# Kernel tuning notes

Hardware: AMD Instinct MI355X
Metric: run time of the kernel (lower is better)

The kernel has to match this reference:

```python
import jax, jax.numpy as jnp
import numpy as np

D = 1024      # model_size
H = 16        # n_heads
HD = D // H   # head_size
B = 8
S = 1024


def setup_inputs() -> dict:
    key = jax.random.key(0)
    ks = jax.random.split(key, 8)
    sq = lambda k, shp: jax.random.normal(k, shp, dtype=jnp.float32) * (1.0 / np.sqrt(shp[0]))
    return {
        "query": jax.random.normal(ks[0], (B, S, D), dtype=jnp.float32),
        "value": jax.random.normal(ks[1], (B, S, D), dtype=jnp.float32),
        "Wq": sq(ks[2], (D, D)),
        "bq": jnp.zeros((D,), dtype=jnp.float32),
        "Wkv": sq(ks[3], (D, 2 * D)),
        "bkv": jnp.zeros((2 * D,), dtype=jnp.float32),
        "Wo": sq(ks[4], (D, D)),
        "bo": jnp.zeros((D,), dtype=jnp.float32),
    }


def reference(query, value, Wq, bq, Wkv, bkv, Wo, bo):
    scale = 1.0 / jnp.sqrt(jnp.float32(HD))
    q = query @ Wq + bq                      # [B,S,D]
    kv = value @ Wkv + bkv                   # [B,S,2D]
    # tf.split(kv, 2H): chunks 0..H-1 are K heads, H..2H-1 are V heads
    k = kv[..., :D].reshape(B, S, H, HD)
    v = kv[..., D:].reshape(B, S, H, HD)
    qh = q.reshape(B, S, H, HD)
    scores = jnp.einsum("bqhd,bkhd->bhqk", qh, k) * scale   # [B,H,S,S]
    attn = jax.nn.softmax(scores, axis=-1)
    heads = jnp.einsum("bhqk,bkhd->bqhd", attn, v).reshape(B, S, D)
    return heads @ Wo + bo
```

## Files before the change

kernel.cpp:

```cpp
#include <hip/hip_runtime.h>
#include <math.h>

#define B_  8
#define S_  1024
#define D_  1024
#define H_  16
#define HD_ 64

typedef float          floatx4  __attribute__((ext_vector_type(4)));
typedef __bf16         bf16x8   __attribute__((ext_vector_type(8)));
typedef unsigned int   uintx2   __attribute__((ext_vector_type(2)));
typedef unsigned int   uintx4   __attribute__((ext_vector_type(4)));

__device__ __forceinline__ unsigned short f2bf(float f) {
    union { float f; unsigned u; } v; v.f = f;
    unsigned r = v.u + 0x7FFFu + ((v.u >> 16) & 1u);
    return (unsigned short)(r >> 16);
}
__device__ __forceinline__ unsigned pk2(float a, float b) {
    union { __bf16 h[2]; unsigned u; } r;
    r.h[0] = (__bf16)a; r.h[1] = (__bf16)b;
    return r.u;
}
__device__ __forceinline__ void async16(const void* g, void* l) {
    __builtin_amdgcn_global_load_lds(
        (__attribute__((address_space(1))) void*)g,
        (__attribute__((address_space(3))) void*)l, 16, 0, 0);
}

__global__ __launch_bounds__(256) void prep_k(const float* __restrict__ query,
                                              const float* __restrict__ value,
                                              unsigned short* __restrict__ qbf,
                                              unsigned short* __restrict__ vbf,
                                              const float* __restrict__ Wq,
                                              const float* __restrict__ Wkv,
                                              const float* __restrict__ Wo,
                                              unsigned short* __restrict__ WqT,
                                              unsigned short* __restrict__ WkvT,
                                              unsigned short* __restrict__ WoT) {
    __shared__ float T[64 * 68];
    const int t   = threadIdx.x;
    const int bid = blockIdx.x;
    if (bid < 8192) {
        int i = bid * 256 + t;
        floatx4 a = ((const floatx4*)query)[i];
        floatx4 b = ((const floatx4*)value)[i];
        uintx2 oa = { pk2(a[0], a[1]), pk2(a[2], a[3]) };
        uintx2 ob = { pk2(b[0], b[1]), pk2(b[2], b[3]) };
        ((uintx2*)qbf)[i] = oa;
        ((uintx2*)vbf)[i] = ob;
        return;
    }
    const int lin = bid - 8192;
    const int z   = lin >> 8;
    const float* W; unsigned short* WT; int Ndim, nbase;
    if (z == 0)      { W = Wq;  WT = WqT;  Ndim = 1024; nbase = 0; }
    else if (z == 3) { W = Wo;  WT = WoT;  Ndim = 1024; nbase = 0; }
    else             { W = Wkv; WT = WkvT; Ndim = 2048; nbase = (z - 1) * 1024; }
    const int n0 = (lin & 15) * 64 + nbase;
    const int k0 = ((lin >> 4) & 15) * 64;
#pragma unroll
    for (int rep = 0; rep < 4; ++rep) {
        int kl = (t >> 4) + rep * 16;
        int ns = (t & 15) * 4;
        *(floatx4*)(T + kl * 68 + ns) = *(const floatx4*)(W + (size_t)(k0 + kl) * Ndim + n0 + ns);
    }
    __syncthreads();
#pragma unroll
    for (int rep = 0; rep < 2; ++rep) {
        int nl = (t >> 3) + rep * 32;
        int ks = (t & 7) * 8;
        union { unsigned short s[8]; uintx4 u; } o;
#pragma unroll
        for (int j = 0; j < 8; ++j) o.s[j] = f2bf(T[(ks + j) * 68 + nl]);
        *(uintx4*)(WT + (size_t)(n0 + nl) * 1024 + k0 + ks) = o.u;
    }
}

template<int SWAP>
__device__ __forceinline__ void kloop(const unsigned short* __restrict__ ga0,
                                      const unsigned short* __restrict__ gb0,
                                      unsigned short* __restrict__ As,
                                      unsigned short* __restrict__ Bs,
                                      floatx4 (&acc)[4][4],
                                      int w, int lane) {
    const int quad = lane >> 4;
    const int l15  = lane & 15;
    const int e7   = l15 & 7;
    const int wr   = (w >> 1) * 64;
    const int wc   = (w & 1) * 64;
    for (int k0 = 0; k0 < 1024; k0 += 64) {
        if (k0) __syncthreads();
#pragma unroll
        for (int i = 0; i < 4; ++i) {
            int c = i * 4 + w;
            async16(ga0 + (size_t)(c * 8) * 1024 + k0, As + c * 512);
            async16(gb0 + (size_t)(c * 8) * 1024 + k0, Bs + c * 512);
        }
        __syncthreads();
#pragma unroll
        for (int ks = 0; ks < 2; ++ks) {
            bf16x8 af[4], bf[4];
#pragma unroll
            for (int mi = 0; mi < 4; ++mi)
                af[mi] = *(const bf16x8*)(As + (wr + mi * 16 + l15) * 64 + (((ks * 4 + quad) ^ e7) * 8));
#pragma unroll
            for (int ni = 0; ni < 4; ++ni)
                bf[ni] = *(const bf16x8*)(Bs + (wc + ni * 16 + l15) * 64 + (((ks * 4 + quad) ^ e7) * 8));
#pragma unroll
            for (int mi = 0; mi < 4; ++mi)
#pragma unroll
                for (int ni = 0; ni < 4; ++ni)
                    acc[mi][ni] = SWAP
                        ? __builtin_amdgcn_mfma_f32_16x16x32_bf16(bf[ni], af[mi], acc[mi][ni], 0, 0, 0)
                        : __builtin_amdgcn_mfma_f32_16x16x32_bf16(af[mi], bf[ni], acc[mi][ni], 0, 0, 0);
        }
    }
}

__global__ __launch_bounds__(256, 4) void qkv_gemm_k(const unsigned short* __restrict__ qbf,
                                                     const unsigned short* __restrict__ vbf,
                                                     const unsigned short* __restrict__ WqT,
                                                     const unsigned short* __restrict__ WkvT,
                                                     const float* __restrict__ bq,
                                                     const float* __restrict__ bkv,
                                                     unsigned short* __restrict__ Qb,
                                                     unsigned short* __restrict__ Kb,
                                                     unsigned short* __restrict__ Vtg,
                                                     float cexp) {
    __shared__ unsigned short SMEM[2 * 128 * 64];
    unsigned short* As = SMEM;
    unsigned short* Bs = SMEM + 128 * 64;
    const int t    = threadIdx.x;
    const int lane = t & 63;
    const int w    = t >> 6;
    const int quad = lane >> 4;
    const int l15  = lane & 15;
    const int wr   = (w >> 1) * 64;
    const int wc   = (w & 1) * 64;
    const int lrow = lane >> 3;
    const int lswz = ((lane & 7) ^ lrow) * 8;

    const int bid = blockIdx.x;
    int m0, n0;
    const unsigned short *Ap, *Wp;
    const float* bp;
    unsigned short* outp;
    float sc;
    bool vpath = false;
    if (bid < 512) {
        m0 = (bid & 63) * 128; n0 = (bid >> 6) * 128;
        Ap = qbf; Wp = WqT; bp = bq; outp = Qb; sc = cexp;
    } else {
        int b2 = bid - 512;
        m0 = (b2 & 63) * 128; n0 = (b2 >> 6) * 128;
        Ap = vbf; Wp = WkvT; bp = bkv; outp = Kb; sc = 1.0f;
        vpath = (n0 >= 1024);
    }

    floatx4 acc[4][4] = {};
    const unsigned short* ga0 = Ap + (size_t)(m0 + lrow) * 1024 + lswz;
    const unsigned short* gb0 = Wp + (size_t)(n0 + lrow) * 1024 + lswz;

    if (!vpath) {
        kloop<1>(ga0, gb0, As, Bs, acc, w, lane);
        __syncthreads();
#pragma unroll
        for (int hn = 0; hn < 2; ++hn) {
            if ((w & 1) == hn) {
#pragma unroll
                for (int ni = 0; ni < 4; ++ni) {
                    const int nb = n0 + wc + ni * 16 + quad * 4;
                    const floatx4 b4 = *(const floatx4*)(bp + nb);
#pragma unroll
                    for (int mi = 0; mi < 4; ++mi) {
                        const int ml = wr + mi * 16 + l15;
                        floatx4 v = acc[mi][ni];
                        uintx2 o = { pk2((v[0] + b4[0]) * sc, (v[1] + b4[1]) * sc),
                                     pk2((v[2] + b4[2]) * sc, (v[3] + b4[3]) * sc) };
                        *(uintx2*)(SMEM + ml * 72 + ni * 16 + quad * 4) = o;
                    }
                }
            }
            __syncthreads();
#pragma unroll
            for (int p = 0; p < 4; ++p) {
                int u   = p * 256 + t;
                int row = u >> 3, ch = u & 7;
                uintx4 x = *(const uintx4*)(SMEM + row * 72 + ch * 8);
                *(uintx4*)(outp + (size_t)(m0 + row) * 1024 + n0 + hn * 64 + ch * 8) = x;
            }
            __syncthreads();
        }
    } else {
        kloop<0>(ga0, gb0, As, Bs, acc, w, lane);
        const int c0 = n0 - 1024;
        const int s0 = m0 & 1023;
        const int bb = m0 >> 10;
        __syncthreads();
#pragma unroll
        for (int hc = 0; hc < 2; ++hc) {
            if ((w & 1) == hc) {
#pragma unroll
                for (int ni = 0; ni < 4; ++ni) {
                    const int rl = ni * 16 + l15;
                    const float bv = bp[n0 + wc + ni * 16 + l15];
#pragma unroll
                    for (int mi = 0; mi < 4; ++mi) {
                        const int sl = wr + mi * 16 + quad * 4;
                        floatx4 v = acc[mi][ni];
                        uintx2 o = { pk2(v[0] + bv, v[1] + bv), pk2(v[2] + bv, v[3] + bv) };
                        *(uintx2*)(SMEM + rl * 136 + sl) = o;
                    }
                }
            }
            __syncthreads();
#pragma unroll
            for (int p = 0; p < 4; ++p) {
                int u   = p * 256 + t;
                int row = u >> 4, ch = u & 15;
                uintx4 x = *(const uintx4*)(SMEM + row * 136 + ch * 8);
                *(uintx4*)(Vtg + ((size_t)(bb * 1024 + c0 + hc * 64 + row)) * 1024 + s0 + ch * 8) = x;
            }
            __syncthreads();
        }
    }
}

__global__ __launch_bounds__(256, 4) void o_gemm_k(const unsigned short* __restrict__ Hb,
                                                   const unsigned short* __restrict__ WoT,
                                                   const float* __restrict__ bo,
                                                   float* __restrict__ out) {
    __shared__ unsigned short As[128 * 64];
    __shared__ unsigned short Bs[128 * 64];
    const int t    = threadIdx.x;
    const int lane = t & 63;
    const int w    = t >> 6;
    const int quad = lane >> 4;
    const int l15  = lane & 15;
    const int wr   = (w >> 1) * 64;
    const int wc   = (w & 1) * 64;
    const int lrow = lane >> 3;
    const int lswz = ((lane & 7) ^ lrow) * 8;
    const int m0   = (blockIdx.x & 63) * 128;
    const int n0   = (blockIdx.x >> 6) * 128;

    floatx4 acc[4][4] = {};
    const unsigned short* ga0 = Hb  + (size_t)(m0 + lrow) * 1024 + lswz;
    const unsigned short* gb0 = WoT + (size_t)(n0 + lrow) * 1024 + lswz;
    kloop<1>(ga0, gb0, As, Bs, acc, w, lane);

#pragma unroll
    for (int ni = 0; ni < 4; ++ni) {
        const int nb = n0 + wc + ni * 16 + quad * 4;
        const floatx4 b4 = *(const floatx4*)(bo + nb);
#pragma unroll
        for (int mi = 0; mi < 4; ++mi) {
            const int m = m0 + wr + mi * 16 + l15;
            floatx4 v = acc[mi][ni];
            floatx4 o = { v[0] + b4[0], v[1] + b4[1], v[2] + b4[2], v[3] + b4[3] };
            *(floatx4*)(out + (size_t)m * 1024 + nb) = o;
        }
    }
}

__global__ __launch_bounds__(256) void attn_kernel(const unsigned short* __restrict__ Qb,
                                                   const unsigned short* __restrict__ Kb,
                                                   const unsigned short* __restrict__ Vtg,
                                                   unsigned short* __restrict__ Hb) {
    __shared__ unsigned short QPs[128 * 64];
    __shared__ unsigned short Ks[2][64 * 64];
    __shared__ unsigned short Vs[2][64 * 64];

    const int lin = blockIdx.x;
    const int xcd = lin & 7;
    const int grp = lin >> 3;
    const int bh  = xcd * 16 + (grp >> 3);
    const int qt  = grp & 7;
    const int b   = bh >> 4;
    const int h   = bh & 15;
    const int q0  = qt * 128;

    const int t    = threadIdx.x;
    const int lane = t & 63;
    const int w    = t >> 6;
    const int quad = lane >> 4;
    const int l15  = lane & 15;
    const int e7   = l15 & 7;
    const int lrow = lane >> 3;
    const int lswz = ((lane & 7) ^ lrow) * 8;

    {
        const unsigned short* gq = Qb + ((size_t)(b * S_ + q0)) * D_ + h * HD_;
#pragma unroll
        for (int i = 0; i < 4; ++i) {
            int r0 = (w * 4 + i) * 8;
            async16(gq + (size_t)(r0 + lrow) * D_ + lswz, QPs + r0 * 64);
        }
    }
    __syncthreads();

    bf16x8 bQ[2][2];
#pragma unroll
    for (int ks = 0; ks < 2; ++ks)
#pragma unroll
        for (int ni = 0; ni < 2; ++ni)
            bQ[ks][ni] = *(const bf16x8*)(QPs + (w * 32 + ni * 16 + l15) * 64 + ((ks * 4 + quad) ^ e7) * 8);

    const unsigned short* gkbase = Kb  + ((size_t)b * S_) * D_ + h * HD_;
    const unsigned short* gvbase = Vtg + ((size_t)(b * D_ + h * HD_)) * S_;

    float   lsum[2] = { 0.f, 0.f };
    floatx4 oacc[4][2] = {};
    unsigned short* Psw = QPs + w * (32 * 64);

    auto stageK = [&](int kt, int buf) {
#pragma unroll
        for (int j = 0; j < 2; ++j) {
            int r0 = (w * 2 + j) * 8;
            async16(gkbase + (size_t)(kt * 64 + r0 + lrow) * D_ + lswz, &Ks[buf][r0 * 64]);
        }
    };
    auto stageV = [&](int kt, int buf) {
#pragma unroll
        for (int j = 0; j < 2; ++j) {
            int r0 = (w * 2 + j) * 8;
            async16(gvbase + (size_t)(r0 + lrow) * S_ + kt * 64 + lswz, &Vs[buf][r0 * 64]);
        }
    };
    auto qk = [&](int buf, floatx4 (&st)[4][2]) {
#pragma unroll
        for (int mi = 0; mi < 4; ++mi)
#pragma unroll
            for (int ni = 0; ni < 2; ++ni)
                st[mi][ni] = floatx4{0.f, 0.f, 0.f, 0.f};
#pragma unroll
        for (int ks = 0; ks < 2; ++ks) {
            bf16x8 aK[4];
#pragma unroll
            for (int mi = 0; mi < 4; ++mi)
                aK[mi] = *(const bf16x8*)(&Ks[buf][0] + (mi * 16 + l15) * 64 + ((ks * 4 + quad) ^ e7) * 8);
            __builtin_amdgcn_s_setprio(1);
#pragma unroll
            for (int mi = 0; mi < 4; ++mi)
#pragma unroll
                for (int ni = 0; ni < 2; ++ni)
                    st[mi][ni] = __builtin_amdgcn_mfma_f32_16x16x32_bf16(aK[mi], bQ[ks][ni], st[mi][ni], 0, 0, 0);
            __builtin_amdgcn_s_setprio(0);
        }
    };

    stageK(0, 0);
    stageK(1, 1);
    stageV(0, 0);
    asm volatile("s_waitcnt vmcnt(4)\n\ts_barrier" ::: "memory");

    floatx4 stA[4][2], stB[4][2];
    qk(0, stA);

    auto body = [&](int kt, floatx4 (&stC)[4][2], floatx4 (&stN)[4][2]) {
        asm volatile("s_waitcnt vmcnt(0)\n\ts_barrier" ::: "memory");
        if (kt < 14) stageK(kt + 2, kt & 1);
        if (kt < 15) stageV(kt + 1, (kt + 1) & 1);

#pragma unroll
        for (int ni = 0; ni < 2; ++ni) {
            float ls = 0.f;
#pragma unroll
            for (int mi = 0; mi < 4; ++mi) {
                float p0 = __builtin_amdgcn_exp2f(stC[mi][ni][0]);
                float p1 = __builtin_amdgcn_exp2f(stC[mi][ni][1]);
                float p2 = __builtin_amdgcn_exp2f(stC[mi][ni][2]);
                float p3 = __builtin_amdgcn_exp2f(stC[mi][ni][3]);
                ls += (p0 + p1) + (p2 + p3);
                uintx2 pk = { pk2(p0, p1), pk2(p2, p3) };
                *(uintx2*)(Psw + (ni * 16 + l15) * 64 +
                           (((2 * mi + (quad >> 1)) ^ e7) * 8 + (quad & 1) * 4)) = pk;
            }
            lsum[ni] += ls;
        }

        if (kt < 15) qk((kt + 1) & 1, stN);

#pragma unroll
        for (int ks = 0; ks < 2; ++ks) {
            bf16x8 aV[4], bP[2];
#pragma unroll
            for (int mi = 0; mi < 4; ++mi)
                aV[mi] = *(const bf16x8*)(&Vs[kt & 1][0] + (mi * 16 + l15) * 64 + ((ks * 4 + quad) ^ e7) * 8);
#pragma unroll
            for (int ni = 0; ni < 2; ++ni)
                bP[ni] = *(const bf16x8*)(Psw + (ni * 16 + l15) * 64 + ((ks * 4 + quad) ^ e7) * 8);
            __builtin_amdgcn_s_setprio(1);
#pragma unroll
            for (int mi = 0; mi < 4; ++mi)
#pragma unroll
                for (int ni = 0; ni < 2; ++ni)
                    oacc[mi][ni] = __builtin_amdgcn_mfma_f32_16x16x32_bf16(aV[mi], bP[ni], oacc[mi][ni], 0, 0, 0);
            __builtin_amdgcn_s_setprio(0);
        }
    };

#pragma unroll 1
    for (int it = 0; it < 8; ++it) {
        body(2 * it,     stA, stB);
        body(2 * it + 1, stB, stA);
    }

    float rl[2];
#pragma unroll
    for (int ni = 0; ni < 2; ++ni) {
        float l = lsum[ni];
        l += __shfl_xor(l, 16);
        l += __shfl_xor(l, 32);
        rl[ni] = 1.f / l;
    }
#pragma unroll
    for (int mi = 0; mi < 4; ++mi)
#pragma unroll
        for (int ni = 0; ni < 2; ++ni) {
            uintx2 pk = { pk2(oacc[mi][ni][0] * rl[ni], oacc[mi][ni][1] * rl[ni]),
                          pk2(oacc[mi][ni][2] * rl[ni], oacc[mi][ni][3] * rl[ni]) };
            *(uintx2*)(Psw + (ni * 16 + l15) * 64 +
                       (((2 * mi + (quad >> 1)) ^ e7) * 8 + (quad & 1) * 4)) = pk;
        }
    {
        int qrow = lane >> 1;
        int kh   = lane & 1;
        size_t obase = ((size_t)(b * S_ + q0 + w * 32 + qrow)) * D_ + h * HD_ + kh * 32;
        int e = qrow & 7;
#pragma unroll
        for (int j = 0; j < 4; ++j) {
            int chunk = kh * 4 + j;
            *(uintx4*)(Hb + obase + j * 8) =
                *(const uintx4*)(Psw + qrow * 64 + ((chunk ^ e) * 8));
        }
    }
}

extern "C" void kernel_launch(void* const* d_in, const int* in_sizes, int n_in,
                              void* d_out, int out_size, void* d_ws, size_t ws_size,
                              hipStream_t stream) {
    (void)in_sizes; (void)n_in; (void)out_size; (void)ws_size;
    const float* query = (const float*)d_in[0];
    const float* value = (const float*)d_in[1];
    const float* Wq    = (const float*)d_in[2];
    const float* bq    = (const float*)d_in[3];
    const float* Wkv   = (const float*)d_in[4];
    const float* bkv   = (const float*)d_in[5];
    const float* Wo    = (const float*)d_in[6];
    const float* bo    = (const float*)d_in[7];

    const size_t MS = (size_t)B_ * S_;
    char* p = (char*)d_ws;
    unsigned short* qbf  = (unsigned short*)p; p += MS * D_ * 2;
    unsigned short* vbf  = (unsigned short*)p; p += MS * D_ * 2;
    unsigned short* WqT  = (unsigned short*)p; p += (size_t)D_ * D_ * 2;
    unsigned short* WkvT = (unsigned short*)p; p += (size_t)2 * D_ * D_ * 2;
    unsigned short* WoT  = (unsigned short*)p; p += (size_t)D_ * D_ * 2;
    unsigned short* Qb   = (unsigned short*)p; p += MS * D_ * 2;
    unsigned short* Kb   = (unsigned short*)p; p += MS * D_ * 2;
    unsigned short* Vtg  = (unsigned short*)p; p += MS * D_ * 2;
    unsigned short* Hb   = qbf;

    const float cexp = 0.125f * 1.44269504088896341f;

    prep_k<<<9216, 256, 0, stream>>>(query, value, qbf, vbf, Wq, Wkv, Wo, WqT, WkvT, WoT);
    qkv_gemm_k<<<1536, 256, 0, stream>>>(qbf, vbf, WqT, WkvT, bq, bkv, Qb, Kb, Vtg, cexp);
    attn_kernel<<<1024, 256, 0, stream>>>(Qb, Kb, Vtg, Hb);
    o_gemm_k<<<512, 256, 0, stream>>>(Hb, WoT, bo, (float*)d_out);
}
```

Measured before the change: 271.7 us.

## Swizzle GEMM block order per XCD and enlarge attention tiles to 256 queries

Measured after the change: 262.8 us. 3.3% less time.

```diff
diff --git a/kernel.cpp b/kernel.cpp
--- a/kernel.cpp
+++ b/kernel.cpp
@@ -141,19 +141,19 @@
     const int lrow = lane >> 3;
     const int lswz = ((lane & 7) ^ lrow) * 8;
 
-    const int bid = blockIdx.x;
+    const int swz = (blockIdx.x & 7) * 192 + (blockIdx.x >> 3);
     int m0, n0;
     const unsigned short *Ap, *Wp;
     const float* bp;
     unsigned short* outp;
     float sc;
     bool vpath = false;
-    if (bid < 512) {
-        m0 = (bid & 63) * 128; n0 = (bid >> 6) * 128;
+    if (swz < 512) {
+        m0 = (swz >> 3) * 128; n0 = (swz & 7) * 128;
         Ap = qbf; Wp = WqT; bp = bq; outp = Qb; sc = cexp;
     } else {
-        int b2 = bid - 512;
-        m0 = (b2 & 63) * 128; n0 = (b2 >> 6) * 128;
+        int b2 = swz - 512;
+        m0 = (b2 >> 4) * 128; n0 = (b2 & 15) * 128;
         Ap = vbf; Wp = WkvT; bp = bkv; outp = Kb; sc = 1.0f;
         vpath = (n0 >= 1024);
     }
@@ -188,7 +188,7 @@
                 int u   = p * 256 + t;
                 int row = u >> 3, ch = u & 7;
                 uintx4 x = *(const uintx4*)(SMEM + row * 72 + ch * 8);
-                *(uintx4*)(outp + (size_t)(m0 + row) * 1024 + n0 + hn * 64 + ch * 8) = x;
+                *(uintx4*)(outp + (size_t)(m0 + row) * 1024 + (n0 & 1023) + hn * 64 + ch * 8) = x;
             }
             __syncthreads();
         }
@@ -242,8 +242,9 @@
     const int wc   = (w & 1) * 64;
     const int lrow = lane >> 3;
     const int lswz = ((lane & 7) ^ lrow) * 8;
-    const int m0   = (blockIdx.x & 63) * 128;
-    const int n0   = (blockIdx.x >> 6) * 128;
+    const int swz = (blockIdx.x & 7) * 64 + (blockIdx.x >> 3);
+    const int m0  = (swz >> 3) * 128;
+    const int n0  = (swz & 7) * 128;
 
     floatx4 acc[4][4] = {};
     const unsigned short* ga0 = Hb  + (size_t)(m0 + lrow) * 1024 + lswz;
@@ -264,22 +265,22 @@
     }
 }
 
-__global__ __launch_bounds__(256) void attn_kernel(const unsigned short* __restrict__ Qb,
-                                                   const unsigned short* __restrict__ Kb,
-                                                   const unsigned short* __restrict__ Vtg,
-                                                   unsigned short* __restrict__ Hb) {
-    __shared__ unsigned short QPs[128 * 64];
+__global__ __launch_bounds__(512, 4) void attn_kernel(const unsigned short* __restrict__ Qb,
+                                                      const unsigned short* __restrict__ Kb,
+                                                      const unsigned short* __restrict__ Vtg,
+                                                      unsigned short* __restrict__ Hb) {
+    __shared__ unsigned short QPs[256 * 64];
     __shared__ unsigned short Ks[2][64 * 64];
     __shared__ unsigned short Vs[2][64 * 64];
 
     const int lin = blockIdx.x;
     const int xcd = lin & 7;
     const int grp = lin >> 3;
-    const int bh  = xcd * 16 + (grp >> 3);
-    const int qt  = grp & 7;
+    const int bh  = xcd * 16 + (grp >> 2);
+    const int qt  = grp & 3;
     const int b   = bh >> 4;
     const int h   = bh & 15;
-    const int q0  = qt * 128;
+    const int q0  = qt * 256;
 
     const int t    = threadIdx.x;
     const int lane = t & 63;
@@ -315,31 +316,30 @@
     unsigned short* Psw = QPs + w * (32 * 64);
 
     auto stageK = [&](int kt, int buf) {
-#pragma unroll
-        for (int j = 0; j < 2; ++j) {
-            int r0 = (w * 2 + j) * 8;
-            async16(gkbase + (size_t)(kt * 64 + r0 + lrow) * D_ + lswz, &Ks[buf][r0 * 64]);
-        }
+        int r0 = w * 8;
+        async16(gkbase + (size_t)(kt * 64 + r0 + lrow) * D_ + lswz, &Ks[buf][r0 * 64]);
     };
     auto stageV = [&](int kt, int buf) {
-#pragma unroll
-        for (int j = 0; j < 2; ++j) {
-            int r0 = (w * 2 + j) * 8;
-            async16(gvbase + (size_t)(r0 + lrow) * S_ + kt * 64 + lswz, &Vs[buf][r0 * 64]);
-        }
+        int r0 = w * 8;
+        async16(gvbase + (size_t)(r0 + lrow) * S_ + kt * 64 + lswz, &Vs[buf][r0 * 64]);
     };
-    auto qk = [&](int buf, floatx4 (&st)[4][2]) {
-#pragma unroll
-        for (int mi = 0; mi < 4; ++mi)
-#pragma unroll
-            for (int ni = 0; ni < 2; ++ni)
-                st[mi][ni] = floatx4{0.f, 0.f, 0.f, 0.f};
+
+    stageK(0, 0);
+    stageV(0, 0);
+
+#pragma unroll 1
+    for (int kt = 0; kt < 16; ++kt) {
+        const int cur = kt & 1;
+        asm volatile("s_waitcnt vmcnt(0)\n\ts_barrier" ::: "memory");
+        if (kt < 15) { stageK(kt + 1, cur ^ 1); stageV(kt + 1, cur ^ 1); }
+
+        floatx4 st[4][2] = {};
 #pragma unroll
         for (int ks = 0; ks < 2; ++ks) {
             bf16x8 aK[4];
 #pragma unroll
             for (int mi = 0; mi < 4; ++mi)
-                aK[mi] = *(const bf16x8*)(&Ks[buf][0] + (mi * 16 + l15) * 64 + ((ks * 4 + quad) ^ e7) * 8);
+                aK[mi] = *(const bf16x8*)(&Ks[cur][0] + (mi * 16 + l15) * 64 + ((ks * 4 + quad) ^ e7) * 8);
             __builtin_amdgcn_s_setprio(1);
 #pragma unroll
             for (int mi = 0; mi < 4; ++mi)
@@ -348,30 +348,16 @@
                     st[mi][ni] = __builtin_amdgcn_mfma_f32_16x16x32_bf16(aK[mi], bQ[ks][ni], st[mi][ni], 0, 0, 0);
             __builtin_amdgcn_s_setprio(0);
         }
-    };
-
-    stageK(0, 0);
-    stageK(1, 1);
-    stageV(0, 0);
-    asm volatile("s_waitcnt vmcnt(4)\n\ts_barrier" ::: "memory");
-
-    floatx4 stA[4][2], stB[4][2];
-    qk(0, stA);
-
-    auto body = [&](int kt, floatx4 (&stC)[4][2], floatx4 (&stN)[4][2]) {
-        asm volatile("s_waitcnt vmcnt(0)\n\ts_barrier" ::: "memory");
-        if (kt < 14) stageK(kt + 2, kt & 1);
-        if (kt < 15) stageV(kt + 1, (kt + 1) & 1);
 
 #pragma unroll
         for (int ni = 0; ni < 2; ++ni) {
             float ls = 0.f;
 #pragma unroll
             for (int mi = 0; mi < 4; ++mi) {
-                float p0 = __builtin_amdgcn_exp2f(stC[mi][ni][0]);
-                float p1 = __builtin_amdgcn_exp2f(stC[mi][ni][1]);
-                float p2 = __builtin_amdgcn_exp2f(stC[mi][ni][2]);
-                float p3 = __builtin_amdgcn_exp2f(stC[mi][ni][3]);
+                float p0 = __builtin_amdgcn_exp2f(st[mi][ni][0]);
+                float p1 = __builtin_amdgcn_exp2f(st[mi][ni][1]);
+                float p2 = __builtin_amdgcn_exp2f(st[mi][ni][2]);
+                float p3 = __builtin_amdgcn_exp2f(st[mi][ni][3]);
                 ls += (p0 + p1) + (p2 + p3);
                 uintx2 pk = { pk2(p0, p1), pk2(p2, p3) };
                 *(uintx2*)(Psw + (ni * 16 + l15) * 64 +
@@ -380,14 +366,12 @@
             lsum[ni] += ls;
         }
 
-        if (kt < 15) qk((kt + 1) & 1, stN);
-
 #pragma unroll
         for (int ks = 0; ks < 2; ++ks) {
             bf16x8 aV[4], bP[2];
 #pragma unroll
             for (int mi = 0; mi < 4; ++mi)
-                aV[mi] = *(const bf16x8*)(&Vs[kt & 1][0] + (mi * 16 + l15) * 64 + ((ks * 4 + quad) ^ e7) * 8);
+                aV[mi] = *(const bf16x8*)(&Vs[cur][0] + (mi * 16 + l15) * 64 + ((ks * 4 + quad) ^ e7) * 8);
 #pragma unroll
             for (int ni = 0; ni < 2; ++ni)
                 bP[ni] = *(const bf16x8*)(Psw + (ni * 16 + l15) * 64 + ((ks * 4 + quad) ^ e7) * 8);
@@ -399,12 +383,6 @@
                     oacc[mi][ni] = __builtin_amdgcn_mfma_f32_16x16x32_bf16(aV[mi], bP[ni], oacc[mi][ni], 0, 0, 0);
             __builtin_amdgcn_s_setprio(0);
         }
-    };
-
-#pragma unroll 1
-    for (int it = 0; it < 8; ++it) {
-        body(2 * it,     stA, stB);
-        body(2 * it + 1, stB, stA);
     }
 
     float rl[2];
@@ -467,6 +445,6 @@
 
     prep_k<<<9216, 256, 0, stream>>>(query, value, qbf, vbf, Wq, Wkv, Wo, WqT, WkvT, WoT);
     qkv_gemm_k<<<1536, 256, 0, stream>>>(qbf, vbf, WqT, WkvT, bq, bkv, Qb, Kb, Vtg, cexp);
-    attn_kernel<<<1024, 256, 0, stream>>>(Qb, Kb, Vtg, Hb);
+    attn_kernel<<<512, 512, 0, stream>>>(Qb, Kb, Vtg, Hb);
     o_gemm_k<<<512, 256, 0, stream>>>(Hb, WoT, bo, (float*)d_out);
 }
```
